# Kernel tuning notes

Hardware: AMD Instinct MI355X
Metric: run time of the kernel (lower is better)

The kernel has to match this reference:

```python
import jax, jax.numpy as jnp
import numpy as np

B, N, C_IN, C_OUT, K = 2, 8192, 128, 128, 21  # K = num_neighbors + 1 (self)
EPS = 1e-5

def knn_idx(xyz, k):
    # xyz: [B,N,3] -> idx [B,N,k] of k nearest neighbors (self included)
    d2 = jnp.sum(xyz * xyz, axis=-1)  # [B,N]
    dist = d2[:, :, None] + d2[:, None, :] - 2.0 * jnp.einsum('bnd,bmd->bnm', xyz, xyz)
    _, idx = jax.lax.top_k(-dist, k)
    return idx

def group_points(pts, idx):
    # pts [B,N,D], idx [B,N,K] -> [B,N,K,D]
    return jax.vmap(lambda p, i: p[i])(pts, idx)

def group_feats(f, idx):
    # f [B,C,N], idx [B,N,K] -> [B,C,N,K]
    return jax.vmap(lambda ff, i: ff[:, i])(f, idx)

def conv_bn_relu(x, W, g, b, m, v):
    # 1x1 conv (bias=False) + BatchNorm (inference stats) + ReLU
    y = jnp.einsum('oc,bcnk->bonk', W, x)
    inv = g / jnp.sqrt(v + EPS)
    return jax.nn.relu(y * inv[None, :, None, None] + (b - m * inv)[None, :, None, None])

def setup_inputs():
    key = jax.random.key(0)
    ks = jax.random.split(key, 12)
    return {
        'xyz': jax.random.normal(ks[0], (B, N, 3), jnp.float32),
        'f': jax.random.normal(ks[1], (B, C_IN, N), jnp.float32),
        'W_geo': jax.random.normal(ks[2], (C_OUT, 6), jnp.float32) * 0.1,
        'g_geo': jax.random.uniform(ks[3], (C_OUT,), jnp.float32, 0.5, 1.5),
        'b_geo': jax.random.normal(ks[4], (C_OUT,), jnp.float32) * 0.1,
        'm_geo': jax.random.normal(ks[5], (C_OUT,), jnp.float32) * 0.1,
        'v_geo': jax.random.uniform(ks[6], (C_OUT,), jnp.float32, 0.5, 1.5),
        'W_feat': jax.random.normal(ks[7], (C_OUT, 2 * C_IN), jnp.float32) * 0.05,
        'g_feat': jax.random.uniform(ks[8], (C_OUT,), jnp.float32, 0.5, 1.5),
        'b_feat': jax.random.normal(ks[9], (C_OUT,), jnp.float32) * 0.1,
        'm_feat': jax.random.normal(ks[10], (C_OUT,), jnp.float32) * 0.1,
        'v_feat': jax.random.uniform(ks[11], (C_OUT,), jnp.float32, 0.5, 1.5),
    }

def reference(xyz, f, W_geo, g_geo, b_geo, m_geo, v_geo, W_feat, g_feat, b_feat, m_feat, v_feat):
    idx = knn_idx(xyz, K)                                   # [B,N,K]
    grouped_xyz = group_points(xyz, idx)                    # [B,N,K,3]
    xyz_diff = jnp.transpose(grouped_xyz - xyz[:, :, None, :], (0, 3, 1, 2))  # [B,3,N,K]
    center = jnp.broadcast_to(jnp.transpose(xyz, (0, 2, 1))[:, :, :, None], (B, 3, N, K))
    G_geo = jnp.concatenate([center, xyz_diff], axis=1)     # [B,6,N,K]
    grouped_f = group_feats(f, idx)                         # [B,C,N,K]
    center_f = jnp.broadcast_to(f[:, :, :, None], (B, C_IN, N, K))
    G_feat = jnp.concatenate([center_f, grouped_f - center_f], axis=1)  # [B,2C,N,K]
    G_geo = conv_bn_relu(G_geo, W_geo, g_geo, b_geo, m_geo, v_geo)      # [B,C_OUT,N,K]
    G_feat = conv_bn_relu(G_feat, W_feat, g_feat, b_feat, m_feat, v_feat)
    feature = jnp.concatenate([G_geo, G_feat], axis=1)      # [B,2*C_OUT,N,K]
    return jnp.max(feature, axis=-1)                        # [B,2*C_OUT,N]
```

## Files before the change

### kernel.cpp

```cpp
#include <hip/hip_runtime.h>

typedef unsigned int u32;
typedef unsigned long long u64;
typedef unsigned short u16;

#define DEV __device__ __forceinline__

DEV u16 f2bf(float x) {
  u32 u = __float_as_uint(x);
  u32 r = u + 0x7fffu + ((u >> 16) & 1u);
  return (u16)(r >> 16);
}
DEV float bflo(u32 d) { return __uint_as_float(d << 16); }
DEV float bfhi(u32 d) { return __uint_as_float(d & 0xffff0000u); }
DEV u64 sortable64(double f) {
  long long b = __double_as_longlong(f);
  return (u64)b ^ (u64)((b >> 63) | (long long)0x8000000000000000ll);
}
DEV double ddist(double qx, double qy, double qz, double qd2,
                 float mxf, float myf, float mzf) {
  double cx = (double)mxf, cy = (double)myf, cz = (double)mzf;
  double cd2 = cx * cx + cy * cy + cz * cz;
  double dot = cx * qx + cy * qy + cz * qz;
  return (qd2 + cd2) - 2.0 * dot;
}

#define NB 2
#define NN 8192
#define NC 128
#define KK 21
#define MARGIN 1e-3f
#define CT 2048

__global__ __launch_bounds__(256) void k_prep(
    const float* __restrict__ Wf, const float* __restrict__ gf, const float* __restrict__ bf_,
    const float* __restrict__ mf, const float* __restrict__ vf,
    const float* __restrict__ Wg, const float* __restrict__ gg, const float* __restrict__ bg,
    const float* __restrict__ mg, const float* __restrict__ vg,
    u16* __restrict__ Wt, float* __restrict__ beta_f,
    float* __restrict__ Wgu, float* __restrict__ Wgv, float* __restrict__ beta_g) {
  int g = blockIdx.x * 256 + threadIdx.x;
  int c = g >> 8, o = g & 255;
  float val;
  if (o < 128) {
    float inv = gf[o] / sqrtf(vf[o] + 1e-5f);
    val = inv * (Wf[o * 256 + c] - Wf[o * 256 + c + 128]);
  } else {
    int o2 = o - 128;
    float inv = gf[o2] / sqrtf(vf[o2] + 1e-5f);
    val = inv * Wf[o2 * 256 + c + 128];
  }
  Wt[c * 256 + o] = f2bf(val);
  if (g < 128) {
    float inv = gf[g] / sqrtf(vf[g] + 1e-5f);
    beta_f[g] = bf_[g] - mf[g] * inv;
  } else if (g < 256) {
    int oo = g - 128;
    float invg = gg[oo] / sqrtf(vg[oo] + 1e-5f);
#pragma unroll
    for (int d = 0; d < 3; ++d) {
      Wgu[oo * 3 + d] = invg * (Wg[oo * 6 + d] - Wg[oo * 6 + 3 + d]);
      Wgv[oo * 3 + d] = invg * Wg[oo * 6 + 3 + d];
    }
    beta_g[oo] = bg[oo] - mg[oo] * invg;
  }
}

__global__ __launch_bounds__(256) void k_geo(
    const float* __restrict__ xyz, const float* __restrict__ Wgu, const float* __restrict__ Wgv,
    const float* __restrict__ beta_g, u32* __restrict__ ucat, u32* __restrict__ vcat) {
  int g = blockIdx.x * 256 + threadIdx.x;
  int p = g >> 6, oc = g & 63;
  const float* xp = xyz + p * 3;
  float X = xp[0], Y = xp[1], Z = xp[2];
  u32 du = 0, dv = 0;
#pragma unroll
  for (int h = 0; h < 2; ++h) {
    int o = oc * 2 + h;
    float ug = X * Wgu[o * 3] + Y * Wgu[o * 3 + 1] + Z * Wgu[o * 3 + 2] + beta_g[o];
    float vv = X * Wgv[o * 3] + Y * Wgv[o * 3 + 1] + Z * Wgv[o * 3 + 2];
    du |= (u32)f2bf(ug) << (16 * h);
    dv |= (u32)f2bf(vv) << (16 * h);
  }
  ucat[p * 128 + oc] = du;
  vcat[p * 128 + oc] = dv;
}

__global__ __launch_bounds__(256) void k_feat(
    const float* __restrict__ f, const u32* __restrict__ Wt32, const float* __restrict__ beta_f,
    u32* __restrict__ ucat, u32* __restrict__ vcat) {
  __shared__ u32 sW[128 * 64];
  __shared__ float sF[128][68];

  const int t = threadIdx.x;
  const int blk = blockIdx.x;
  const int H = blk & 1;
  const int b = blk >> 8;
  const int n0 = ((blk >> 1) & 127) << 6;
  const int boff = b * (NC * NN);

#pragma unroll
  for (int k = 0; k < 32; ++k) {
    int i = t + (k << 8);
    sW[i] = Wt32[((i >> 6) << 7) + (H << 6) + (i & 63)];
  }
#pragma unroll
  for (int k = 0; k < 32; ++k) {
    int i = t + (k << 8);
    int c = i >> 6, col = i & 63;
    sF[c][col] = f[boff + c * NN + n0 + col];
  }
  __syncthreads();

  const int w = t >> 6, lane = t & 63;
  const int og = lane >> 4, pg = lane & 15;
  const int o0 = (w << 5) + (og << 3);
  const int p0 = pg << 2;

  float acc[8][4];
#pragma unroll
  for (int a = 0; a < 8; ++a)
#pragma unroll
    for (int p = 0; p < 4; ++p) acc[a][p] = 0.0f;

  for (int c = 0; c < 128; ++c) {
    float4 fa = *(const float4*)&sF[c][p0];
    uint4 wr = *(const uint4*)&sW[(c << 6) + (o0 >> 1)];
    float wv[8] = {bflo(wr.x), bfhi(wr.x), bflo(wr.y), bfhi(wr.y),
                   bflo(wr.z), bfhi(wr.z), bflo(wr.w), bfhi(wr.w)};
    float fv[4] = {fa.x, fa.y, fa.z, fa.w};
#pragma unroll
    for (int a = 0; a < 8; ++a)
#pragma unroll
      for (int p = 0; p < 4; ++p) acc[a][p] = __builtin_fmaf(wv[a], fv[p], acc[a][p]);
  }

  float bet[8];
#pragma unroll
  for (int a = 0; a < 8; ++a) bet[a] = (H == 0) ? beta_f[o0 + a] : 0.0f;
  u32* dstbase = (H == 0) ? ucat : vcat;
#pragma unroll
  for (int p = 0; p < 4; ++p) {
    int pt = (b << 13) + n0 + p0 + p;
    u32 d0 = (u32)f2bf(acc[0][p] + bet[0]) | ((u32)f2bf(acc[1][p] + bet[1]) << 16);
    u32 d1 = (u32)f2bf(acc[2][p] + bet[2]) | ((u32)f2bf(acc[3][p] + bet[3]) << 16);
    u32 d2 = (u32)f2bf(acc[4][p] + bet[4]) | ((u32)f2bf(acc[5][p] + bet[5]) << 16);
    u32 d3 = (u32)f2bf(acc[6][p] + bet[6]) | ((u32)f2bf(acc[7][p] + bet[7]) << 16);
    *(uint4*)&dstbase[pt * 128 + 64 + (o0 >> 1)] = make_uint4(d0, d1, d2, d3);
  }
}

__global__ __launch_bounds__(256) void k_knn(const float* __restrict__ xyz,
                                             int* __restrict__ knn) {
  __shared__ float4 sc[CT];
  __shared__ u16 ssurv[16][128];
  __shared__ u32 scnt[16];

  const int t = threadIdx.x;
  const int blk = blockIdx.x;
  const int b = blk >> 9;
  const int n0 = (blk & 511) << 4;
  const float* X = xyz + b * (NN * 3);

  if (t < 16) scnt[t] = 0u;

  const int w = t >> 6, lane = t & 63;

  float mx[4], my[4], mz[4];
#pragma unroll
  for (int i = 0; i < 4; ++i) {
    int q = n0 + (w << 2) + i;
    mx[i] = -2.0f * X[q * 3];
    my[i] = -2.0f * X[q * 3 + 1];
    mz[i] = -2.0f * X[q * 3 + 2];
  }

  float px[8], py[8], pz[8];
#pragma unroll
  for (int k = 0; k < 8; ++k) {
    int c = (k << 8) + t;
    px[k] = X[c * 3]; py[k] = X[c * 3 + 1]; pz[k] = X[c * 3 + 2];
  }

  float mn[4];
#pragma unroll
  for (int i = 0; i < 4; ++i) mn[i] = __builtin_inff();

  for (int ct = 0; ct < NN / CT; ++ct) {
    __syncthreads();
#pragma unroll
    for (int k = 0; k < 8; ++k) {
      int c = (k << 8) + t;
      float x = px[k], y = py[k], z = pz[k];
      sc[c] = make_float4(x, y, z, __builtin_fmaf(x, x, __builtin_fmaf(y, y, z * z)));
    }
    if (ct < NN / CT - 1) {
      const float* Xt = X + (ct + 1) * (CT * 3);
#pragma unroll
      for (int k = 0; k < 8; ++k) {
        int c = (k << 8) + t;
        px[k] = Xt[c * 3]; py[k] = Xt[c * 3 + 1]; pz[k] = Xt[c * 3 + 2];
      }
    }
    __syncthreads();
#pragma unroll 4
    for (int cc = 0; cc < CT; cc += 64) {
      float4 C = sc[cc + lane];
#pragma unroll
      for (int i = 0; i < 4; ++i) {
        float s = __builtin_fmaf(C.x, mx[i],
                  __builtin_fmaf(C.y, my[i],
                  __builtin_fmaf(C.z, mz[i], C.w)));
        mn[i] = fminf(mn[i], s);
      }
    }
  }

#pragma unroll
  for (int k = 0; k < 8; ++k) {
    int c = (k << 8) + t;
    px[k] = X[c * 3]; py[k] = X[c * 3 + 1]; pz[k] = X[c * 3 + 2];
  }

  float thr[4];
#pragma unroll
  for (int i = 0; i < 4; ++i) {
    float v = mn[i];
#pragma unroll
    for (int k = 2; k <= 64; k <<= 1) {
#pragma unroll
      for (int j = k >> 1; j > 0; j >>= 1) {
        float p = __shfl_xor(v, j);
        bool takeMin = (((lane & k) == 0) == ((lane & j) == 0));
        v = takeMin ? fminf(v, p) : fmaxf(v, p);
      }
    }
    thr[i] = __shfl(v, 20) + MARGIN;
  }

  for (int ct = 0; ct < NN / CT; ++ct) {
    __syncthreads();
#pragma unroll
    for (int k = 0; k < 8; ++k) {
      int c = (k << 8) + t;
      float x = px[k], y = py[k], z = pz[k];
      sc[c] = make_float4(x, y, z, __builtin_fmaf(x, x, __builtin_fmaf(y, y, z * z)));
    }
    if (ct < NN / CT - 1) {
      const float* Xt = X + (ct + 1) * (CT * 3);
#pragma unroll
      for (int k = 0; k < 8; ++k) {
        int c = (k << 8) + t;
        px[k] = Xt[c * 3]; py[k] = Xt[c * 3 + 1]; pz[k] = Xt[c * 3 + 2];
      }
    }
    __syncthreads();
    int mbase = ct * CT + lane;
#pragma unroll 4
    for (int cc = 0; cc < CT; cc += 64) {
      float4 C = sc[cc + lane];
#pragma unroll
      for (int i = 0; i < 4; ++i) {
        float s = __builtin_fmaf(C.x, mx[i],
                  __builtin_fmaf(C.y, my[i],
                  __builtin_fmaf(C.z, mz[i], C.w)));
        if (s <= thr[i]) {
          int qq = (w << 2) + i;
          u32 slot = atomicAdd(&scnt[qq], 1u);
          if (slot < 128u) ssurv[qq][slot] = (u16)(mbase + cc);
        }
      }
    }
  }
  __syncthreads();

#pragma unroll 1
  for (int i = 0; i < 4; ++i) {
    const int qq = (w << 2) + i;
    const int q = n0 + qq;
    double Qx = (double)X[q * 3], Qy = (double)X[q * 3 + 1], Qz = (double)X[q * 3 + 2];
    double Qd2 = Qx * Qx + Qy * Qy + Qz * Qz;
    u32 cnt = scnt[qq];
    int* outp = knn + ((b << 13) + q) * KK;

    bool v0 = ((u32)lane < cnt);
    u32 m0 = v0 ? (u32)ssurv[qq][lane] : 0u;
    double s0 = ddist(Qx, Qy, Qz, Qd2, X[m0 * 3], X[m0 * 3 + 1], X[m0 * 3 + 2]);
    u64 k0 = v0 ? ((sortable64(s0) & 0xFFFFFFFFFFFFE000ull) | (u64)m0) : ~0ull;

    if (cnt <= 64u) {
      u64 v = k0;
#pragma unroll
      for (int k = 2; k <= 64; k <<= 1) {
#pragma unroll
        for (int j = k >> 1; j > 0; j >>= 1) {
          u64 p = __shfl_xor(v, j);
          bool takeMin = (((lane & k) == 0) == ((lane & j) == 0));
          bool pl = p < v;
          u64 mnv = pl ? p : v;
          u64 mxv = pl ? v : p;
          v = takeMin ? mnv : mxv;
        }
      }
      if (lane < KK) outp[lane] = (int)(v & 8191ull);
    } else {
      bool v1 = ((u32)(lane + 64) < cnt);
      u32 m1 = v1 ? (u32)ssurv[qq][lane + 64] : 0u;
      double s1 = ddist(Qx, Qy, Qz, Qd2, X[m1 * 3], X[m1 * 3 + 1], X[m1 * 3 + 2]);
      u64 k1 = v1 ? ((sortable64(s1) & 0xFFFFFFFFFFFFE000ull) | (u64)m1) : ~0ull;
      u32 selm = 0;
      for (int r = 0; r < KK; ++r) {
        u64 mk = (k0 < k1) ? k0 : k1;
#pragma unroll
        for (int j = 32; j > 0; j >>= 1) {
          u64 p = __shfl_xor(mk, j);
          if (p < mk) mk = p;
        }
        if (k0 == mk) k0 = ~0ull;
        else if (k1 == mk) k1 = ~0ull;
        if (lane == r) selm = (u32)(mk & 8191ull);
      }
      if (lane < KK) outp[lane] = (int)selm;
    }
  }
}

__global__ __launch_bounds__(256) void k_gather(
    const u32* __restrict__ ucat, const u32* __restrict__ vcat,
    const int* __restrict__ knn, float* __restrict__ out) {
  __shared__ float tr[64 * 65];

  const int t = threadIdx.x;
  const int blk = blockIdx.x;
  const int Q = blk & 3;
  const int b = blk >> 9;
  const int n0 = ((blk >> 2) & 127) << 6;
  const int w = t >> 6, lane = t & 63;
  const int half = lane >> 5;
  const int l32 = lane & 31;
  const int lo = (Q << 5) | l32;

  for (int step = 0; step < 8; ++step) {
    int qq = (step << 3) + (w << 1) + half;
    int q = n0 + qq;
    const int* ip = knn + ((b << 13) + q) * KK;
    float a0 = -__builtin_inff(), a1 = -__builtin_inff();
#pragma unroll
    for (int k = 0; k < KK; ++k) {
      int p = ip[k];
      u32 d = vcat[(((b << 13) + p) << 7) + lo];
      a0 = fmaxf(a0, bflo(d));
      a1 = fmaxf(a1, bfhi(d));
    }
    u32 u = ucat[(((b << 13) + q) << 7) + lo];
    tr[qq * 65 + l32] = fmaxf(bflo(u) + a0, 0.0f);
    tr[qq * 65 + 32 + l32] = fmaxf(bfhi(u) + a1, 0.0f);
  }
  __syncthreads();

  float* ob = out + b * (256 * NN) + (Q << 6) * NN;
  for (int i = 0; i < 16; ++i) {
    int o = (w << 4) + i;
    int col = ((o & 1) << 5) + (o >> 1);
    ob[o * NN + n0 + lane] = tr[lane * 65 + col];
  }
}

extern "C" void kernel_launch(void* const* d_in, const int* in_sizes, int n_in,
                              void* d_out, int out_size, void* d_ws, size_t ws_size,
                              hipStream_t stream) {
  const float* xyz = (const float*)d_in[0];
  const float* f   = (const float*)d_in[1];
  const float* Wg  = (const float*)d_in[2];
  const float* gg  = (const float*)d_in[3];
  const float* bg  = (const float*)d_in[4];
  const float* mg  = (const float*)d_in[5];
  const float* vg  = (const float*)d_in[6];
  const float* Wf  = (const float*)d_in[7];
  const float* gf  = (const float*)d_in[8];
  const float* bf_ = (const float*)d_in[9];
  const float* mf  = (const float*)d_in[10];
  const float* vf  = (const float*)d_in[11];

  char* ws = (char*)d_ws;
  u16*   Wt     = (u16*)ws;
  float* beta_f = (float*)(ws + 65536);
  float* Wgu    = (float*)(ws + 66048);
  float* Wgv    = (float*)(ws + 67584);
  float* beta_g = (float*)(ws + 69120);
  u32*   ucat   = (u32*)(ws + 69632);
  u32*   vcat   = (u32*)(ws + 69632 + 8388608);
  int*   knn    = (int*)(ws + 69632 + 2 * 8388608);
  float* out    = (float*)d_out;

  if (ws_size < (size_t)(69632 + 2 * 8388608 + 16384 * KK * 4)) return;

  k_prep<<<dim3(128), dim3(256), 0, stream>>>(Wf, gf, bf_, mf, vf, Wg, gg, bg, mg, vg,
                                              Wt, beta_f, Wgu, Wgv, beta_g);
  k_geo<<<dim3(4096), dim3(256), 0, stream>>>(xyz, Wgu, Wgv, beta_g, ucat, vcat);
  k_feat<<<dim3(512), dim3(256), 0, stream>>>(f, (const u32*)Wt, beta_f, ucat, vcat);
  k_knn<<<dim3(1024), dim3(256), 0, stream>>>(xyz, knn);
  k_gather<<<dim3(1024), dim3(256), 0, stream>>>(ucat, vcat, knn, out);
}
```

Baseline: 187.4 us.

## Merge prep into KNN kernel with full-cloud LDS staging, fuse feat and geo kernels

Folds the weight-prep work into extra blocks of the KNN kernel. The KNN kernel now uses 1024-thread blocks covering 64 queries each and stages the whole 8192-point cloud (128 KB) in shared memory once, instead of streaming 2048-point tiles twice. The feature GEMM and geometric projection kernels become one launch with a block-index split, cutting the launch count from five to three. Tradeoffs: 128 KB of LDS per block limits occupancy to about one block per CU, and the atomic counter contention pattern for survivor slots changes.

```diff
diff --git a/kernel.cpp b/kernel.cpp
--- a/kernel.cpp
+++ b/kernel.cpp
@@ -30,139 +30,56 @@
 #define NC 128
 #define KK 21
 #define MARGIN 1e-3f
-#define CT 2048
-
-__global__ __launch_bounds__(256) void k_prep(
+
+__global__ __launch_bounds__(1024) void k_knnprep(
+    const float* __restrict__ xyz, int* __restrict__ knn,
     const float* __restrict__ Wf, const float* __restrict__ gf, const float* __restrict__ bf_,
     const float* __restrict__ mf, const float* __restrict__ vf,
     const float* __restrict__ Wg, const float* __restrict__ gg, const float* __restrict__ bg,
     const float* __restrict__ mg, const float* __restrict__ vg,
     u16* __restrict__ Wt, float* __restrict__ beta_f,
     float* __restrict__ Wgu, float* __restrict__ Wgv, float* __restrict__ beta_g) {
-  int g = blockIdx.x * 256 + threadIdx.x;
-  int c = g >> 8, o = g & 255;
-  float val;
-  if (o < 128) {
-    float inv = gf[o] / sqrtf(vf[o] + 1e-5f);
-    val = inv * (Wf[o * 256 + c] - Wf[o * 256 + c + 128]);
-  } else {
-    int o2 = o - 128;
-    float inv = gf[o2] / sqrtf(vf[o2] + 1e-5f);
-    val = inv * Wf[o2 * 256 + c + 128];
-  }
-  Wt[c * 256 + o] = f2bf(val);
-  if (g < 128) {
-    float inv = gf[g] / sqrtf(vf[g] + 1e-5f);
-    beta_f[g] = bf_[g] - mf[g] * inv;
-  } else if (g < 256) {
-    int oo = g - 128;
-    float invg = gg[oo] / sqrtf(vg[oo] + 1e-5f);
-#pragma unroll
-    for (int d = 0; d < 3; ++d) {
-      Wgu[oo * 3 + d] = invg * (Wg[oo * 6 + d] - Wg[oo * 6 + 3 + d]);
-      Wgv[oo * 3 + d] = invg * Wg[oo * 6 + 3 + d];
-    }
-    beta_g[oo] = bg[oo] - mg[oo] * invg;
-  }
-}
-
-__global__ __launch_bounds__(256) void k_geo(
-    const float* __restrict__ xyz, const float* __restrict__ Wgu, const float* __restrict__ Wgv,
-    const float* __restrict__ beta_g, u32* __restrict__ ucat, u32* __restrict__ vcat) {
-  int g = blockIdx.x * 256 + threadIdx.x;
-  int p = g >> 6, oc = g & 63;
-  const float* xp = xyz + p * 3;
-  float X = xp[0], Y = xp[1], Z = xp[2];
-  u32 du = 0, dv = 0;
-#pragma unroll
-  for (int h = 0; h < 2; ++h) {
-    int o = oc * 2 + h;
-    float ug = X * Wgu[o * 3] + Y * Wgu[o * 3 + 1] + Z * Wgu[o * 3 + 2] + beta_g[o];
-    float vv = X * Wgv[o * 3] + Y * Wgv[o * 3 + 1] + Z * Wgv[o * 3 + 2];
-    du |= (u32)f2bf(ug) << (16 * h);
-    dv |= (u32)f2bf(vv) << (16 * h);
-  }
-  ucat[p * 128 + oc] = du;
-  vcat[p * 128 + oc] = dv;
-}
-
-__global__ __launch_bounds__(256) void k_feat(
-    const float* __restrict__ f, const u32* __restrict__ Wt32, const float* __restrict__ beta_f,
-    u32* __restrict__ ucat, u32* __restrict__ vcat) {
-  __shared__ u32 sW[128 * 64];
-  __shared__ float sF[128][68];
+  __shared__ float4 sc[NN];
+  __shared__ u16 ssurv[64][128];
+  __shared__ u32 scnt[64];
 
   const int t = threadIdx.x;
-  const int blk = blockIdx.x;
-  const int H = blk & 1;
-  const int b = blk >> 8;
-  const int n0 = ((blk >> 1) & 127) << 6;
-  const int boff = b * (NC * NN);
-
-#pragma unroll
-  for (int k = 0; k < 32; ++k) {
-    int i = t + (k << 8);
-    sW[i] = Wt32[((i >> 6) << 7) + (H << 6) + (i & 63)];
-  }
-#pragma unroll
-  for (int k = 0; k < 32; ++k) {
-    int i = t + (k << 8);
-    int c = i >> 6, col = i & 63;
-    sF[c][col] = f[boff + c * NN + n0 + col];
-  }
-  __syncthreads();
-
-  const int w = t >> 6, lane = t & 63;
-  const int og = lane >> 4, pg = lane & 15;
-  const int o0 = (w << 5) + (og << 3);
-  const int p0 = pg << 2;
-
-  float acc[8][4];
-#pragma unroll
-  for (int a = 0; a < 8; ++a)
-#pragma unroll
-    for (int p = 0; p < 4; ++p) acc[a][p] = 0.0f;
-
-  for (int c = 0; c < 128; ++c) {
-    float4 fa = *(const float4*)&sF[c][p0];
-    uint4 wr = *(const uint4*)&sW[(c << 6) + (o0 >> 1)];
-    float wv[8] = {bflo(wr.x), bfhi(wr.x), bflo(wr.y), bfhi(wr.y),
-                   bflo(wr.z), bfhi(wr.z), bflo(wr.w), bfhi(wr.w)};
-    float fv[4] = {fa.x, fa.y, fa.z, fa.w};
-#pragma unroll
-    for (int a = 0; a < 8; ++a)
-#pragma unroll
-      for (int p = 0; p < 4; ++p) acc[a][p] = __builtin_fmaf(wv[a], fv[p], acc[a][p]);
-  }
-
-  float bet[8];
-#pragma unroll
-  for (int a = 0; a < 8; ++a) bet[a] = (H == 0) ? beta_f[o0 + a] : 0.0f;
-  u32* dstbase = (H == 0) ? ucat : vcat;
-#pragma unroll
-  for (int p = 0; p < 4; ++p) {
-    int pt = (b << 13) + n0 + p0 + p;
-    u32 d0 = (u32)f2bf(acc[0][p] + bet[0]) | ((u32)f2bf(acc[1][p] + bet[1]) << 16);
-    u32 d1 = (u32)f2bf(acc[2][p] + bet[2]) | ((u32)f2bf(acc[3][p] + bet[3]) << 16);
-    u32 d2 = (u32)f2bf(acc[4][p] + bet[4]) | ((u32)f2bf(acc[5][p] + bet[5]) << 16);
-    u32 d3 = (u32)f2bf(acc[6][p] + bet[6]) | ((u32)f2bf(acc[7][p] + bet[7]) << 16);
-    *(uint4*)&dstbase[pt * 128 + 64 + (o0 >> 1)] = make_uint4(d0, d1, d2, d3);
-  }
-}
-
-__global__ __launch_bounds__(256) void k_knn(const float* __restrict__ xyz,
-                                             int* __restrict__ knn) {
-  __shared__ float4 sc[CT];
-  __shared__ u16 ssurv[16][128];
-  __shared__ u32 scnt[16];
-
-  const int t = threadIdx.x;
-  const int blk = blockIdx.x;
-  const int b = blk >> 9;
-  const int n0 = (blk & 511) << 4;
+
+  if (blockIdx.x < 32) {
+    int g = (blockIdx.x << 10) + t;
+    int c = g >> 8, o = g & 255;
+    float val;
+    if (o < 128) {
+      float inv = gf[o] / sqrtf(vf[o] + 1e-5f);
+      val = inv * (Wf[o * 256 + c] - Wf[o * 256 + c + 128]);
+    } else {
+      int o2 = o - 128;
+      float inv = gf[o2] / sqrtf(vf[o2] + 1e-5f);
+      val = inv * Wf[o2 * 256 + c + 128];
+    }
+    Wt[c * 256 + o] = f2bf(val);
+    if (g < 128) {
+      float inv = gf[g] / sqrtf(vf[g] + 1e-5f);
+      beta_f[g] = bf_[g] - mf[g] * inv;
+    } else if (g < 256) {
+      int oo = g - 128;
+      float invg = gg[oo] / sqrtf(vg[oo] + 1e-5f);
+#pragma unroll
+      for (int d = 0; d < 3; ++d) {
+        Wgu[oo * 3 + d] = invg * (Wg[oo * 6 + d] - Wg[oo * 6 + 3 + d]);
+        Wgv[oo * 3 + d] = invg * Wg[oo * 6 + 3 + d];
+      }
+      beta_g[oo] = bg[oo] - mg[oo] * invg;
+    }
+    return;
+  }
+
+  const int kb = blockIdx.x - 32;
+  const int b = kb >> 7;
+  const int n0 = (kb & 127) << 6;
   const float* X = xyz + b * (NN * 3);
 
-  if (t < 16) scnt[t] = 0u;
+  if (t < 64) scnt[t] = 0u;
 
   const int w = t >> 6, lane = t & 63;
 
@@ -175,51 +92,29 @@
     mz[i] = -2.0f * X[q * 3 + 2];
   }
 
-  float px[8], py[8], pz[8];
 #pragma unroll
   for (int k = 0; k < 8; ++k) {
-    int c = (k << 8) + t;
-    px[k] = X[c * 3]; py[k] = X[c * 3 + 1]; pz[k] = X[c * 3 + 2];
-  }
+    int c = (k << 10) + t;
+    float x = X[c * 3], y = X[c * 3 + 1], z = X[c * 3 + 2];
+    float d2 = __builtin_fmaf(x, x, __builtin_fmaf(y, y, z * z));
+    sc[c] = make_float4(x, y, z, d2);
+  }
+  __syncthreads();
 
   float mn[4];
 #pragma unroll
   for (int i = 0; i < 4; ++i) mn[i] = __builtin_inff();
 
-  for (int ct = 0; ct < NN / CT; ++ct) {
-    __syncthreads();
-#pragma unroll
-    for (int k = 0; k < 8; ++k) {
-      int c = (k << 8) + t;
-      float x = px[k], y = py[k], z = pz[k];
-      sc[c] = make_float4(x, y, z, __builtin_fmaf(x, x, __builtin_fmaf(y, y, z * z)));
-    }
-    if (ct < NN / CT - 1) {
-      const float* Xt = X + (ct + 1) * (CT * 3);
-#pragma unroll
-      for (int k = 0; k < 8; ++k) {
-        int c = (k << 8) + t;
-        px[k] = Xt[c * 3]; py[k] = Xt[c * 3 + 1]; pz[k] = Xt[c * 3 + 2];
-      }
-    }
-    __syncthreads();
 #pragma unroll 4
-    for (int cc = 0; cc < CT; cc += 64) {
-      float4 C = sc[cc + lane];
-#pragma unroll
-      for (int i = 0; i < 4; ++i) {
-        float s = __builtin_fmaf(C.x, mx[i],
-                  __builtin_fmaf(C.y, my[i],
-                  __builtin_fmaf(C.z, mz[i], C.w)));
-        mn[i] = fminf(mn[i], s);
-      }
-    }
-  }
-
-#pragma unroll
-  for (int k = 0; k < 8; ++k) {
-    int c = (k << 8) + t;
-    px[k] = X[c * 3]; py[k] = X[c * 3 + 1]; pz[k] = X[c * 3 + 2];
+  for (int cc = 0; cc < NN; cc += 64) {
+    float4 C = sc[cc + lane];
+#pragma unroll
+    for (int i = 0; i < 4; ++i) {
+      float s = __builtin_fmaf(C.x, mx[i],
+                __builtin_fmaf(C.y, my[i],
+                __builtin_fmaf(C.z, mz[i], C.w)));
+      mn[i] = fminf(mn[i], s);
+    }
   }
 
   float thr[4];
@@ -238,37 +133,19 @@
     thr[i] = __shfl(v, 20) + MARGIN;
   }
 
-  for (int ct = 0; ct < NN / CT; ++ct) {
-    __syncthreads();
-#pragma unroll
-    for (int k = 0; k < 8; ++k) {
-      int c = (k << 8) + t;
-      float x = px[k], y = py[k], z = pz[k];
-      sc[c] = make_float4(x, y, z, __builtin_fmaf(x, x, __builtin_fmaf(y, y, z * z)));
-    }
-    if (ct < NN / CT - 1) {
-      const float* Xt = X + (ct + 1) * (CT * 3);
-#pragma unroll
-      for (int k = 0; k < 8; ++k) {
-        int c = (k << 8) + t;
-        px[k] = Xt[c * 3]; py[k] = Xt[c * 3 + 1]; pz[k] = Xt[c * 3 + 2];
-      }
-    }
-    __syncthreads();
-    int mbase = ct * CT + lane;
-#pragma unroll 4
-    for (int cc = 0; cc < CT; cc += 64) {
-      float4 C = sc[cc + lane];
-#pragma unroll
-      for (int i = 0; i < 4; ++i) {
-        float s = __builtin_fmaf(C.x, mx[i],
-                  __builtin_fmaf(C.y, my[i],
-                  __builtin_fmaf(C.z, mz[i], C.w)));
-        if (s <= thr[i]) {
-          int qq = (w << 2) + i;
-          u32 slot = atomicAdd(&scnt[qq], 1u);
-          if (slot < 128u) ssurv[qq][slot] = (u16)(mbase + cc);
-        }
+#pragma unroll 2
+  for (int cc = 0; cc < NN; cc += 64) {
+    float4 C = sc[cc + lane];
+    int mbase = cc + lane;
+#pragma unroll
+    for (int i = 0; i < 4; ++i) {
+      float s = __builtin_fmaf(C.x, mx[i],
+                __builtin_fmaf(C.y, my[i],
+                __builtin_fmaf(C.z, mz[i], C.w)));
+      if (s <= thr[i]) {
+        int qq = (w << 2) + i;
+        u32 slot = atomicAdd(&scnt[qq], 1u);
+        if (slot < 128u) ssurv[qq][slot] = (u16)mbase;
       }
     }
   }
@@ -322,6 +199,91 @@
       }
       if (lane < KK) outp[lane] = (int)selm;
     }
+  }
+}
+
+__global__ __launch_bounds__(256) void k_featgeo(
+    const float* __restrict__ f, const u32* __restrict__ Wt32, const float* __restrict__ beta_f,
+    const float* __restrict__ xyz, const float* __restrict__ Wgu, const float* __restrict__ Wgv,
+    const float* __restrict__ beta_g, u32* __restrict__ ucat, u32* __restrict__ vcat) {
+  __shared__ u32 sW[128 * 64];
+  __shared__ float sF[128][68];
+
+  const int t = threadIdx.x;
+
+  if (blockIdx.x >= 512) {
+    int g = ((blockIdx.x - 512) << 8) + t;
+    int p = g >> 6, oc = g & 63;
+    const float* xp = xyz + p * 3;
+    float X = xp[0], Y = xp[1], Z = xp[2];
+    u32 du = 0, dv = 0;
+#pragma unroll
+    for (int h = 0; h < 2; ++h) {
+      int o = oc * 2 + h;
+      float ug = X * Wgu[o * 3] + Y * Wgu[o * 3 + 1] + Z * Wgu[o * 3 + 2] + beta_g[o];
+      float vv = X * Wgv[o * 3] + Y * Wgv[o * 3 + 1] + Z * Wgv[o * 3 + 2];
+      du |= (u32)f2bf(ug) << (16 * h);
+      dv |= (u32)f2bf(vv) << (16 * h);
+    }
+    ucat[p * 128 + oc] = du;
+    vcat[p * 128 + oc] = dv;
+    return;
+  }
+
+  const int blk = blockIdx.x;
+  const int H = blk & 1;
+  const int b = blk >> 8;
+  const int n0 = ((blk >> 1) & 127) << 6;
+  const int boff = b * (NC * NN);
+
+#pragma unroll
+  for (int k = 0; k < 32; ++k) {
+    int i = t + (k << 8);
+    sW[i] = Wt32[((i >> 6) << 7) + (H << 6) + (i & 63)];
+  }
+#pragma unroll
+  for (int k = 0; k < 32; ++k) {
+    int i = t + (k << 8);
+    int c = i >> 6, col = i & 63;
+    sF[c][col] = f[boff + c * NN + n0 + col];
+  }
+  __syncthreads();
+
+  const int w = t >> 6, lane = t & 63;
+  const int og = lane >> 4, pg = lane & 15;
+  const int o0 = (w << 5) + (og << 3);
+  const int p0 = pg << 2;
+
+  float acc[8][4];
+#pragma unroll
+  for (int a = 0; a < 8; ++a)
+#pragma unroll
+    for (int p = 0; p < 4; ++p) acc[a][p] = 0.0f;
+
+  for (int c = 0; c < 128; ++c) {
+    float4 fa = *(const float4*)&sF[c][p0];
+    uint4 wr = *(const uint4*)&sW[(c << 6) + (o0 >> 1)];
+    float wv[8] = {bflo(wr.x), bfhi(wr.x), bflo(wr.y), bfhi(wr.y),
+                   bflo(wr.z), bfhi(wr.z), bflo(wr.w), bfhi(wr.w)};
+    float fv[4] = {fa.x, fa.y, fa.z, fa.w};
+#pragma unroll
+    for (int a = 0; a < 8; ++a)
+#pragma unroll
+      for (int p = 0; p < 4; ++p) acc[a][p] = __builtin_fmaf(wv[a], fv[p], acc[a][p]);
+  }
+
+  float bet[8];
+#pragma unroll
+  for (int a = 0; a < 8; ++a) bet[a] = (H == 0) ? beta_f[o0 + a] : 0.0f;
+  u32* dstbase = (H == 0) ? ucat : vcat;
+#pragma unroll
+  for (int p = 0; p < 4; ++p) {
+    int pt = (b << 13) + n0 + p0 + p;
+    u32 d0 = (u32)f2bf(acc[0][p] + bet[0]) | ((u32)f2bf(acc[1][p] + bet[1]) << 16);
+    u32 d1 = (u32)f2bf(acc[2][p] + bet[2]) | ((u32)f2bf(acc[3][p] + bet[3]) << 16);
+    u32 d2 = (u32)f2bf(acc[4][p] + bet[4]) | ((u32)f2bf(acc[5][p] + bet[5]) << 16);
+    u32 d3 = (u32)f2bf(acc[6][p] + bet[6]) | ((u32)f2bf(acc[7][p] + bet[7]) << 16);
+    *(uint4*)&dstbase[pt * 128 + 64 + (o0 >> 1)] = make_uint4(d0, d1, d2, d3);
   }
 }
 
@@ -395,10 +357,10 @@
 
   if (ws_size < (size_t)(69632 + 2 * 8388608 + 16384 * KK * 4)) return;
 
-  k_prep<<<dim3(128), dim3(256), 0, stream>>>(Wf, gf, bf_, mf, vf, Wg, gg, bg, mg, vg,
-                                              Wt, beta_f, Wgu, Wgv, beta_g);
-  k_geo<<<dim3(4096), dim3(256), 0, stream>>>(xyz, Wgu, Wgv, beta_g, ucat, vcat);
-  k_feat<<<dim3(512), dim3(256), 0, stream>>>(f, (const u32*)Wt, beta_f, ucat, vcat);
-  k_knn<<<dim3(1024), dim3(256), 0, stream>>>(xyz, knn);
+  k_knnprep<<<dim3(288), dim3(1024), 0, stream>>>(
+      xyz, knn, Wf, gf, bf_, mf, vf, Wg, gg, bg, mg, vg,
+      Wt, beta_f, Wgu, Wgv, beta_g);
+  k_featgeo<<<dim3(4608), dim3(256), 0, stream>>>(
+      f, (const u32*)Wt, beta_f, xyz, Wgu, Wgv, beta_g, ucat, vcat);
   k_gather<<<dim3(1024), dim3(256), 0, stream>>>(ucat, vcat, knn, out);
 }
```

After: 175.3 us. -6.5%, faster.
